# Kernel optimization log

Measured on AMD Instinct MI355X. Metric: run time of the kernel, lower is better.

The kernel has to match this reference:

```python
import jax, jax.numpy as jnp
import numpy as np

B, S, H = 2, 2048, 2048
NQ, NKV, D = 16, 4, 128
GROUPS = NQ // NKV
SCALE = 1.0 / np.sqrt(D).astype(np.float32)


def _make_rope(seq_len, dim, dtype=jnp.float32):
    inv_freq = 1.0 / (10000.0 ** (jnp.arange(0, dim, 2, dtype=jnp.float32) / dim))
    t = jnp.arange(seq_len, dtype=jnp.float32)
    freqs = jnp.outer(t, inv_freq)                      # [S, D/2]
    emb = jnp.concatenate([freqs, freqs], axis=-1)      # [S, D]
    cos = jnp.cos(emb).astype(dtype)[None, :, None, :]  # [1, S, 1, D]
    sin = jnp.sin(emb).astype(dtype)[None, :, None, :]
    return jnp.broadcast_to(cos, (B, seq_len, 1, dim)), jnp.broadcast_to(sin, (B, seq_len, 1, dim))


def _rotate_half(x):
    x1, x2 = jnp.split(x, 2, axis=-1)
    return jnp.concatenate([-x2, x1], axis=-1)


def _apply_rope(x, cos, sin):
    # x: [B, S, Hh, D]; cos/sin: [B, S, 1, D]
    return x * cos + _rotate_half(x) * sin


def setup_inputs() -> dict:
    key = jax.random.key(0)
    ks = jax.random.split(key, 8)
    x = jax.random.normal(ks[0], (B, S, H), dtype=jnp.float32)
    rope_cos, rope_sin = _make_rope(S, D)
    std = 1.0 / np.sqrt(H)
    Wq = jax.random.normal(ks[1], (NQ * D, H), dtype=jnp.float32) * std
    bq = jax.random.normal(ks[2], (NQ * D,), dtype=jnp.float32) * 0.01
    Wk = jax.random.normal(ks[3], (NKV * D, H), dtype=jnp.float32) * std
    bk = jax.random.normal(ks[4], (NKV * D,), dtype=jnp.float32) * 0.01
    Wv = jax.random.normal(ks[5], (NKV * D, H), dtype=jnp.float32) * std
    bv = jax.random.normal(ks[6], (NKV * D,), dtype=jnp.float32) * 0.01
    Wo = jax.random.normal(ks[7], (H, NQ * D), dtype=jnp.float32) * (1.0 / np.sqrt(NQ * D))
    return {"x": x, "rope_cos": rope_cos, "rope_sin": rope_sin,
            "Wq": Wq, "bq": bq, "Wk": Wk, "bk": bk, "Wv": Wv, "bv": bv, "Wo": Wo}


def reference(x, rope_cos, rope_sin, Wq, bq, Wk, bk, Wv, bv, Wo):
    Bx, Sx, _ = x.shape
    q = (x @ Wq.T + bq).reshape(Bx, Sx, NQ, D)
    k = (x @ Wk.T + bk).reshape(Bx, Sx, NKV, D)
    v = (x @ Wv.T + bv).reshape(Bx, Sx, NKV, D)
    q = _apply_rope(q, rope_cos, rope_sin)
    k = _apply_rope(k, rope_cos, rope_sin)
    q = q.transpose(0, 2, 1, 3)   # [B, NQ, S, D]
    k = k.transpose(0, 2, 1, 3)   # [B, NKV, S, D]
    v = v.transpose(0, 2, 1, 3)
    new_k, new_v = k, v           # kv cache (pre-repeat)
    kr = jnp.repeat(k, GROUPS, axis=1)  # [B, NQ, S_k, D]
    vr = jnp.repeat(v, GROUPS, axis=1)
    S_k = kr.shape[2]
    attn = jnp.einsum('bhsd,bhtd->bhst', q, kr) * SCALE
    row = jnp.arange(Sx)[:, None] + (S_k - Sx)
    col = jnp.arange(S_k)[None, :]
    mask = col > row                       # [S, S_k]
    attn = jnp.where(mask[None, None], -jnp.inf, attn)
    attn_max = jnp.max(attn, axis=-1, keepdims=True)
    attn = jnp.exp(attn - attn_max)
    attn = attn / (jnp.sum(attn, axis=-1, keepdims=True) + 1e-9)
    attn = jnp.nan_to_num(attn, nan=0.0)
    out = jnp.einsum('bhst,bhtd->bhsd', attn, vr)
    out = out.transpose(0, 2, 1, 3).reshape(Bx, Sx, NQ * D)
    out = out @ Wo.T
    return (out, new_k, new_v)
```

## Files before the change

kernel.cpp:

```cpp
#include <hip/hip_runtime.h>
#include <cstdint>
#include <cstddef>
#include <math.h>

constexpr int Bc   = 2;
constexpr int Sc   = 2048;
constexpr int Hc   = 2048;
constexpr int NQc  = 16;
constexpr int NKVc = 4;
constexpr int Dc   = 128;
#define SCALE_F 0.08838834764831845f

typedef __attribute__((ext_vector_type(8))) short  bf16x8;
typedef __attribute__((ext_vector_type(4))) float  f32x4;
typedef __attribute__((ext_vector_type(16))) float f32x16;

__device__ __forceinline__ uint16_t f2bf(float f) {
    union { float f; uint32_t u; } v; v.f = f;
    uint32_t u = v.u;
    return (uint16_t)((u + 0x7FFFu + ((u >> 16) & 1u)) >> 16);
}
__device__ __forceinline__ uint32_t pk2bf(float lo, float hi) {
    return (uint32_t)f2bf(lo) | ((uint32_t)f2bf(hi) << 16);
}
__device__ __forceinline__ float bfu2f(uint16_t u) {
    union { uint32_t u; float f; } v; v.u = (uint32_t)u << 16; return v.f;
}
__device__ __forceinline__ void lds_load16(void* lds, const void* g) {
    __builtin_amdgcn_global_load_lds(
        (const __attribute__((address_space(1))) uint32_t*)g,
        (__attribute__((address_space(3))) uint32_t*)lds, 16, 0, 0);
}
__device__ __forceinline__ bf16x8 mk8(uint32_t w0, uint32_t w1, uint32_t w2, uint32_t w3) {
    union { uint32_t u[4]; bf16x8 s; } t;
    t.u[0] = w0; t.u[1] = w1; t.u[2] = w2; t.u[3] = w3; return t.s;
}

__global__ __launch_bounds__(256) void cvt1_kernel(
    const float* __restrict__ x,  const float* __restrict__ wq,
    const float* __restrict__ wk, const float* __restrict__ wv,
    uint16_t* __restrict__ xb, uint16_t* __restrict__ wqkv)
{
    const long long TOT = 3670016LL;
    for (long long i = (long long)blockIdx.x * 256 + threadIdx.x; i < TOT;
         i += (long long)gridDim.x * 256) {
        const float* src; uint16_t* dst; long long off;
        if (i < 2097152LL)      { src = x;  dst = xb;             off = i; }
        else if (i < 3145728LL) { src = wq; dst = wqkv;           off = i - 2097152LL; }
        else if (i < 3407872LL) { src = wk; dst = wqkv + 4194304; off = i - 3145728LL; }
        else                    { src = wv; dst = wqkv + 5242880; off = i - 3407872LL; }
        float4 v = *((const float4*)src + off);
        uint2 o; o.x = pk2bf(v.x, v.y); o.y = pk2bf(v.z, v.w);
        *((uint2*)dst + off) = o;
    }
}

__global__ __launch_bounds__(256) void cvt2_kernel(
    const float* __restrict__ wo, uint16_t* __restrict__ wob)
{
    for (long long i = (long long)blockIdx.x * 256 + threadIdx.x; i < 1048576LL;
         i += (long long)gridDim.x * 256) {
        float4 v = *((const float4*)wo + i);
        uint2 o; o.x = pk2bf(v.x, v.y); o.y = pk2bf(v.z, v.w);
        *((uint2*)wob + i) = o;
    }
}

__device__ __forceinline__ void gemm_stage(const uint16_t* __restrict__ src,
                                           size_t row_stride, uint16_t* lds,
                                           int wid, int lane)
{
    #pragma unroll
    for (int i = 0; i < 4; ++i) {
        const int g = wid * 4 + i;
        const int r = g * 8 + (lane >> 3);
        const int slot = (lane & 7) ^ (r & 7);
        lds_load16(lds + g * 512, src + (size_t)r * row_stride + slot * 8);
    }
}

#define GEMM_CORE(AS, BS, AB, BB)                                              \
    f32x4 acc[4][4] = {};                                                      \
    gemm_stage(AB, 2048, &AS[0][0], wid, lane);                                \
    gemm_stage(BB, 2048, &BS[0][0], wid, lane);                                \
    __syncthreads();                                                           \
    for (int t = 0; t < 32; ++t) {                                             \
        const int cur = t & 1;                                                 \
        if (t + 1 < 32) {                                                      \
            gemm_stage(AB + (t + 1) * 64, 2048, &AS[cur ^ 1][0], wid, lane);   \
            gemm_stage(BB + (t + 1) * 64, 2048, &BS[cur ^ 1][0], wid, lane);   \
        }                                                                      \
        _Pragma("unroll")                                                      \
        for (int kk = 0; kk < 2; ++kk) {                                       \
            bf16x8 av[4], bw[4];                                               \
            _Pragma("unroll")                                                  \
            for (int mi = 0; mi < 4; ++mi) {                                   \
                const int row = wr * 64 + mi * 16 + (lane & 15);               \
                const int slot = (kk * 4 + (lane >> 4)) ^ (row & 7);           \
                av[mi] = *(const bf16x8*)&AS[cur][row * 64 + slot * 8];        \
            }                                                                  \
            _Pragma("unroll")                                                  \
            for (int nj = 0; nj < 4; ++nj) {                                   \
                const int row = wc * 64 + nj * 16 + (lane & 15);               \
                const int slot = (kk * 4 + (lane >> 4)) ^ (row & 7);           \
                bw[nj] = *(const bf16x8*)&BS[cur][row * 64 + slot * 8];        \
            }                                                                  \
            _Pragma("unroll")                                                  \
            for (int mi = 0; mi < 4; ++mi)                                     \
                _Pragma("unroll")                                              \
                for (int nj = 0; nj < 4; ++nj)                                 \
                    acc[mi][nj] = __builtin_amdgcn_mfma_f32_16x16x32_bf16(     \
                        av[mi], bw[nj], acc[mi][nj], 0, 0, 0);                 \
        }                                                                      \
        __syncthreads();                                                       \
    }

__global__ __launch_bounds__(256) void gemm_qkv_kernel(
    const uint16_t* __restrict__ xb, const uint16_t* __restrict__ wqkv,
    const float* __restrict__ bq, const float* __restrict__ bk, const float* __restrict__ bv,
    uint16_t* __restrict__ qb2, float* __restrict__ kbuf, float* __restrict__ vbuf)
{
    __shared__ __align__(16) uint16_t As[2][128 * 64];
    __shared__ __align__(16) uint16_t Bs[2][128 * 64];
    const int tid = threadIdx.x, lane = tid & 63, wid = tid >> 6;
    const int m0 = blockIdx.x * 128, n0 = blockIdx.y * 128;
    const int wr = wid >> 1, wc = wid & 1;
    const uint16_t* Ab = xb + (size_t)m0 * 2048;
    const uint16_t* Bb = wqkv + (size_t)n0 * 2048;

    GEMM_CORE(As, Bs, Ab, Bb)

    const float* bias; int rtype; int nbase;
    if (n0 < 2048)      { bias = bq + n0;          rtype = 0; nbase = n0; }
    else if (n0 < 2560) { bias = bk + (n0 - 2048); rtype = 1; nbase = n0 - 2048; }
    else                { bias = bv + (n0 - 2560); rtype = 2; nbase = n0 - 2560; }
    #pragma unroll
    for (int mi = 0; mi < 4; ++mi) {
        #pragma unroll
        for (int nj = 0; nj < 4; ++nj) {
            const int ct = wc * 64 + nj * 16 + (lane & 15);
            const int nloc = nbase + ct;
            const int head = nloc >> 7, d = nloc & 127;
            const float bval = bias[ct];
            #pragma unroll
            for (int j = 0; j < 4; ++j) {
                const int m = m0 + wr * 64 + mi * 16 + (lane >> 4) * 4 + j;
                const int bb2 = m >> 11, ss = m & 2047;
                const float v = acc[mi][nj][j] + bval;
                if (rtype == 0)
                    qb2[(((size_t)(bb2 * NQc + head) * Sc) + ss) * Dc + d] = f2bf(v);
                else if (rtype == 1)
                    kbuf[(((size_t)(bb2 * NKVc + head) * Sc) + ss) * Dc + d] = v;
                else
                    vbuf[(((size_t)(bb2 * NKVc + head) * Sc) + ss) * Dc + d] = v;
            }
        }
    }
}

__global__ __launch_bounds__(256) void gemm_out_kernel(
    const uint16_t* __restrict__ ab, const uint16_t* __restrict__ wob,
    float* __restrict__ C)
{
    __shared__ __align__(16) uint16_t As[2][128 * 64];
    __shared__ __align__(16) uint16_t Bs[2][128 * 64];
    const int tid = threadIdx.x, lane = tid & 63, wid = tid >> 6;
    const int m0 = blockIdx.x * 128, n0 = blockIdx.y * 128;
    const int wr = wid >> 1, wc = wid & 1;
    const uint16_t* Ab = ab + (size_t)m0 * 2048;
    const uint16_t* Bb = wob + (size_t)n0 * 2048;

    GEMM_CORE(As, Bs, Ab, Bb)

    #pragma unroll
    for (int mi = 0; mi < 4; ++mi) {
        #pragma unroll
        for (int nj = 0; nj < 4; ++nj) {
            const int n = n0 + wc * 64 + nj * 16 + (lane & 15);
            #pragma unroll
            for (int j = 0; j < 4; ++j) {
                const int m = m0 + wr * 64 + mi * 16 + (lane >> 4) * 4 + j;
                C[(size_t)m * 2048 + n] = acc[mi][nj][j];
            }
        }
    }
}

__global__ __launch_bounds__(256) void rope_kernel(
    uint16_t* __restrict__ qb2, float* __restrict__ kbuf,
    const float* __restrict__ cosb, const float* __restrict__ sinb,
    uint16_t* __restrict__ kb2)
{
    const int idx = blockIdx.x * 256 + threadIdx.x;
    const int e = idx & 31;
    int t = idx >> 5;
    const int ss = t & 2047; t >>= 11;
    const int h = t % 20, bb = t / 20;
    const float* cp = cosb + ((size_t)bb * Sc + ss) * Dc;
    const float* sp = sinb + ((size_t)bb * Sc + ss) * Dc;
    const float2 c1 = *(const float2*)(cp + 2 * e);
    const float2 c2 = *(const float2*)(cp + 64 + 2 * e);
    const float2 s1 = *(const float2*)(sp + 2 * e);
    const float2 s2 = *(const float2*)(sp + 64 + 2 * e);
    if (h < NQc) {
        const size_t base = (((size_t)(bb * NQc + h) * Sc) + ss) * Dc;
        const uint32_t u1 = *(const uint32_t*)(qb2 + base + 2 * e);
        const uint32_t u2 = *(const uint32_t*)(qb2 + base + 64 + 2 * e);
        const float x1a = bfu2f((uint16_t)u1), x1b = bfu2f((uint16_t)(u1 >> 16));
        const float x2a = bfu2f((uint16_t)u2), x2b = bfu2f((uint16_t)(u2 >> 16));
        const float lo0 = x1a * c1.x - x2a * s1.x, lo1 = x1b * c1.y - x2b * s1.y;
        const float hi0 = x2a * c2.x + x1a * s2.x, hi1 = x2b * c2.y + x1b * s2.y;
        *(uint32_t*)(qb2 + base + 2 * e)      = pk2bf(lo0, lo1);
        *(uint32_t*)(qb2 + base + 64 + 2 * e) = pk2bf(hi0, hi1);
    } else {
        const int hh = h - NQc;
        const size_t base = (((size_t)(bb * NKVc + hh) * Sc) + ss) * Dc;
        const float2 x1 = *(const float2*)(kbuf + base + 2 * e);
        const float2 x2 = *(const float2*)(kbuf + base + 64 + 2 * e);
        const float lo0 = x1.x * c1.x - x2.x * s1.x, lo1 = x1.y * c1.y - x2.y * s1.y;
        const float hi0 = x2.x * c2.x + x1.x * s2.x, hi1 = x2.y * c2.y + x1.y * s2.y;
        *(float2*)(kbuf + base + 2 * e)      = make_float2(lo0, lo1);
        *(float2*)(kbuf + base + 64 + 2 * e) = make_float2(hi0, hi1);
        *(uint32_t*)(kb2 + base + 2 * e)      = pk2bf(lo0, lo1);
        *(uint32_t*)(kb2 + base + 64 + 2 * e) = pk2bf(hi0, hi1);
    }
}

__global__ __launch_bounds__(256) void vtrans_kernel(
    const float* __restrict__ vbuf, uint16_t* __restrict__ vt)
{
    __shared__ uint16_t T[128][72];
    const int tid = threadIdx.x;
    const int st = blockIdx.x & 31;
    const int bh = blockIdx.x >> 5;
    const float* src = vbuf + ((size_t)bh * Sc + st * 64) * Dc;
    #pragma unroll
    for (int i = 0; i < 8; ++i) {
        const int f = tid + 256 * i;
        const int s_l = f >> 5, d4 = (f & 31) * 4;
        const float4 v = *((const float4*)(src + (size_t)s_l * Dc) + (f & 31));
        T[d4 + 0][s_l] = f2bf(v.x); T[d4 + 1][s_l] = f2bf(v.y);
        T[d4 + 2][s_l] = f2bf(v.z); T[d4 + 3][s_l] = f2bf(v.w);
    }
    __syncthreads();
    uint16_t* dst = vt + (size_t)bh * Dc * Sc + st * 64;
    #pragma unroll
    for (int i = 0; i < 8; ++i) {
        const int g = tid + 256 * i;
        const int d = g >> 4, s4 = (g & 15) * 4;
        *(uint2*)(dst + (size_t)d * Sc + s4) = *(const uint2*)&T[d][s4];
    }
}

__global__ __launch_bounds__(256, 2) void attn_kernel(
    const uint16_t* __restrict__ qb, const uint16_t* __restrict__ kb,
    const uint16_t* __restrict__ vt, uint16_t* __restrict__ ab)
{
    __shared__ __align__(16) uint16_t Ks[2][64 * 128];
    __shared__ __align__(16) uint16_t Vs[2][128 * 64];

    const int tid = threadIdx.x, lane = tid & 63, wid = tid >> 6;
    const int qt = 15 - blockIdx.x;
    const int bh = blockIdx.y;
    const int b = bh >> 4, h = bh & 15, hk = h >> 2;
    const int l31 = lane & 31, l5 = lane >> 5;

    const uint16_t* kpB = kb + ((size_t)(b * NKVc + hk) * Sc) * Dc;
    const uint16_t* vpB = vt + ((size_t)(b * NKVc + hk) * Dc) * Sc;

    const uint16_t* qbase =
        qb + (((size_t)(b * NQc + h) * Sc) + qt * 128 + wid * 32 + l31) * Dc;
    bf16x8 qf[8];
    #pragma unroll
    for (int kk = 0; kk < 8; ++kk)
        qf[kk] = *(const bf16x8*)(qbase + kk * 16 + l5 * 8);

    float m_r = -INFINITY, l_r = 0.f;
    f32x16 o0 = {}, o1 = {}, o2 = {}, o3 = {};

    const int qg = qt * 128 + wid * 32 + l31;
    const int NCH = 2 * qt + 2;

    auto stage = [&](int ch, int buf) {
        const int kb0 = ch * 64;
        #pragma unroll
        for (int i = 0; i < 4; ++i) {
            const int g = wid * 4 + i;
            const int row = g * 4 + (lane >> 4);
            const int slot = (lane & 15) ^ (row & 15);
            lds_load16(&Ks[buf][g * 512], kpB + (size_t)(kb0 + row) * Dc + slot * 8);
        }
        #pragma unroll
        for (int i = 0; i < 4; ++i) {
            const int g = wid * 4 + i;
            const int d = g * 8 + (lane >> 3);
            const int slot = (lane & 7) ^ (d & 7);
            lds_load16(&Vs[buf][g * 512], vpB + (size_t)d * Sc + kb0 + slot * 8);
        }
    };

    stage(0, 0);
    __syncthreads();

    for (int ch = 0; ch < NCH; ++ch) {
        const int buf = ch & 1;
        if (ch + 1 < NCH) stage(ch + 1, buf ^ 1);
        const int kb0 = ch * 64;

        f32x16 s0 = {}, s1 = {};
        #pragma unroll
        for (int kk = 0; kk < 8; ++kk) {
            const int r0 = l31;
            const int sl0 = (kk * 2 + l5) ^ (r0 & 15);
            const bf16x8 a0 = *(const bf16x8*)&Ks[buf][r0 * 128 + sl0 * 8];
            const int r1 = 32 + l31;
            const int sl1 = (kk * 2 + l5) ^ (r1 & 15);
            const bf16x8 a1 = *(const bf16x8*)&Ks[buf][r1 * 128 + sl1 * 8];
            s0 = __builtin_amdgcn_mfma_f32_32x32x16_bf16(a0, qf[kk], s0, 0, 0, 0);
            s1 = __builtin_amdgcn_mfma_f32_32x32x16_bf16(a1, qf[kk], s1, 0, 0, 0);
        }

        float p[32];
        float rm = -INFINITY;
        #pragma unroll
        for (int r = 0; r < 16; ++r) {
            const int krel = (r & 3) + 8 * (r >> 2) + 4 * l5;
            float v0 = s0[r] * SCALE_F;
            float v1 = s1[r] * SCALE_F;
            if (kb0 + krel > qg)      v0 = -INFINITY;
            if (kb0 + 32 + krel > qg) v1 = -INFINITY;
            p[r] = v0; p[16 + r] = v1;
            rm = fmaxf(rm, fmaxf(v0, v1));
        }
        rm = fmaxf(rm, __shfl_xor(rm, 32));
        const float mnew = fmaxf(m_r, rm);
        const float alpha = __expf(m_r - mnew);
        m_r = mnew;

        float sum = 0.f;
        uint32_t pb[16];
        #pragma unroll
        for (int j = 0; j < 8; ++j) {
            const float a0 = __expf(p[2 * j] - mnew),      a1 = __expf(p[2 * j + 1] - mnew);
            const float b0 = __expf(p[16 + 2 * j] - mnew), b1 = __expf(p[16 + 2 * j + 1] - mnew);
            sum += (a0 + a1) + (b0 + b1);
            pb[j]     = pk2bf(a0, a1);
            pb[8 + j] = pk2bf(b0, b1);
        }
        sum += __shfl_xor(sum, 32);
        l_r = l_r * alpha + sum;

        #pragma unroll
        for (int r = 0; r < 16; ++r) {
            const int qi = (r & 3) + 8 * (r >> 2) + 4 * l5;
            const float av = __shfl(alpha, qi);
            o0[r] *= av; o1[r] *= av; o2[r] *= av; o3[r] *= av;
        }

        uint32_t e[16];
        #pragma unroll
        for (int j = 0; j < 16; ++j) e[j] = __shfl_xor(pb[j], 32);
        const bool hi = (l5 == 1);
        const bf16x8 pa0 = hi ? mk8(e[2],  e[3],  pb[2],  pb[3])  : mk8(pb[0],  pb[1],  e[0],  e[1]);
        const bf16x8 pa1 = hi ? mk8(e[6],  e[7],  pb[6],  pb[7])  : mk8(pb[4],  pb[5],  e[4],  e[5]);
        const bf16x8 pa2 = hi ? mk8(e[10], e[11], pb[10], pb[11]) : mk8(pb[8],  pb[9],  e[8],  e[9]);
        const bf16x8 pa3 = hi ? mk8(e[14], e[15], pb[14], pb[15]) : mk8(pb[12], pb[13], e[12], e[13]);

        #define PV_DV(OO, DV)                                                        \
        {                                                                            \
            const int d = (DV) * 32 + l31;                                           \
            const int rb = d * 64; const int sw = d & 7;                             \
            const bf16x8 b0 = *(const bf16x8*)&Vs[buf][rb + ((0 * 2 + l5) ^ sw) * 8];\
            OO = __builtin_amdgcn_mfma_f32_32x32x16_bf16(pa0, b0, OO, 0, 0, 0);      \
            const bf16x8 b1 = *(const bf16x8*)&Vs[buf][rb + ((1 * 2 + l5) ^ sw) * 8];\
            OO = __builtin_amdgcn_mfma_f32_32x32x16_bf16(pa1, b1, OO, 0, 0, 0);      \
            const bf16x8 b2 = *(const bf16x8*)&Vs[buf][rb + ((2 * 2 + l5) ^ sw) * 8];\
            OO = __builtin_amdgcn_mfma_f32_32x32x16_bf16(pa2, b2, OO, 0, 0, 0);      \
            const bf16x8 b3 = *(const bf16x8*)&Vs[buf][rb + ((3 * 2 + l5) ^ sw) * 8];\
            OO = __builtin_amdgcn_mfma_f32_32x32x16_bf16(pa3, b3, OO, 0, 0, 0);      \
        }
        PV_DV(o0, 0) PV_DV(o1, 1) PV_DV(o2, 2) PV_DV(o3, 3)
        #undef PV_DV

        __syncthreads();
    }

    const float inv = 1.f / (l_r + 1e-9f);
    uint16_t* abase = ab + ((size_t)b * Sc) * 2048 + (size_t)h * Dc;
    #pragma unroll
    for (int r = 0; r < 16; ++r) {
        const int qi = (r & 3) + 8 * (r >> 2) + 4 * l5;
        const float iv = __shfl(inv, qi);
        const int srow = qt * 128 + wid * 32 + qi;
        uint16_t* dst = abase + (size_t)srow * 2048 + l31;
        dst[0]  = f2bf(o0[r] * iv);
        dst[32] = f2bf(o1[r] * iv);
        dst[64] = f2bf(o2[r] * iv);
        dst[96] = f2bf(o3[r] * iv);
    }
}

extern "C" void kernel_launch(void* const* d_in, const int* in_sizes, int n_in,
                              void* d_out, int out_size, void* d_ws, size_t ws_size,
                              hipStream_t stream)
{
    const float* x    = (const float*)d_in[0];
    const float* cosb = (const float*)d_in[1];
    const float* sinb = (const float*)d_in[2];
    const float* Wq   = (const float*)d_in[3];
    const float* bq   = (const float*)d_in[4];
    const float* Wk   = (const float*)d_in[5];
    const float* bk   = (const float*)d_in[6];
    const float* Wv   = (const float*)d_in[7];
    const float* bv   = (const float*)d_in[8];
    const float* Wo   = (const float*)d_in[9];

    float* out  = (float*)d_out;
    float* kout = out  + (size_t)Bc * Sc * Hc;
    float* vout = kout + (size_t)Bc * NKVc * Sc * Dc;
    uint16_t* qb2 = (uint16_t*)out;

    uint8_t* ws = (uint8_t*)d_ws;
    uint16_t* xb   = (uint16_t*)(ws);
    uint16_t* wqkv = (uint16_t*)(ws + (16u << 20));
    uint16_t* kb2  = (uint16_t*)(ws + (16u << 20));
    uint16_t* vb2t = (uint16_t*)(ws + (20u << 20));
    uint16_t* wob  = (uint16_t*)(ws + (24u << 20));
    uint16_t* ab   = (uint16_t*)(ws);

    cvt1_kernel<<<2048, 256, 0, stream>>>(x, Wq, Wk, Wv, xb, wqkv);

    gemm_qkv_kernel<<<dim3(32, 24), 256, 0, stream>>>(xb, wqkv, bq, bk, bv,
                                                      qb2, kout, vout);

    rope_kernel<<<10240, 256, 0, stream>>>(qb2, kout, cosb, sinb, kb2);

    vtrans_kernel<<<256, 256, 0, stream>>>(vout, vb2t);

    cvt2_kernel<<<1024, 256, 0, stream>>>(Wo, wob);

    attn_kernel<<<dim3(16, 32), 256, 0, stream>>>(qb2, kb2, vb2t, ab);

    gemm_out_kernel<<<dim3(32, 16), 256, 0, stream>>>(ab, wob, out);
}
```

Baseline: 381.4 us.

## Skip fully masked per-wave chunks, lazy rescale, exp2 softmax, permlane swap in attention

```diff
diff --git a/kernel.cpp b/kernel.cpp
--- a/kernel.cpp
+++ b/kernel.cpp
@@ -260,8 +260,10 @@
     __shared__ __align__(16) uint16_t Vs[2][128 * 64];
 
     const int tid = threadIdx.x, lane = tid & 63, wid = tid >> 6;
-    const int qt = 15 - blockIdx.x;
-    const int bh = blockIdx.y;
+    const int lin = blockIdx.x;
+    const int hf = lin >> 8, pp = lin & 255;
+    const int qt = hf ? (pp & 15) : (15 - (pp & 15));
+    const int bh = (pp >> 4) + hf * 16;
     const int b = bh >> 4, h = bh & 15, hk = h >> 2;
     const int l31 = lane & 31, l5 = lane >> 5;
 
@@ -278,8 +280,11 @@
     float m_r = -INFINITY, l_r = 0.f;
     f32x16 o0 = {}, o1 = {}, o2 = {}, o3 = {};
 
-    const int qg = qt * 128 + wid * 32 + l31;
+    const int qg      = qt * 128 + wid * 32 + l31;
+    const int qgw_min = qt * 128 + wid * 32;
+    const int qgw_max = qgw_min + 31;
     const int NCH = 2 * qt + 2;
+    constexpr float SCL2 = 0.08838834764831845f * 1.4426950408889634f;
 
     auto stage = [&](int ch, int buf) {
         const int kb0 = ch * 64;
@@ -307,80 +312,107 @@
         if (ch + 1 < NCH) stage(ch + 1, buf ^ 1);
         const int kb0 = ch * 64;
 
-        f32x16 s0 = {}, s1 = {};
-        #pragma unroll
-        for (int kk = 0; kk < 8; ++kk) {
-            const int r0 = l31;
-            const int sl0 = (kk * 2 + l5) ^ (r0 & 15);
-            const bf16x8 a0 = *(const bf16x8*)&Ks[buf][r0 * 128 + sl0 * 8];
-            const int r1 = 32 + l31;
-            const int sl1 = (kk * 2 + l5) ^ (r1 & 15);
-            const bf16x8 a1 = *(const bf16x8*)&Ks[buf][r1 * 128 + sl1 * 8];
-            s0 = __builtin_amdgcn_mfma_f32_32x32x16_bf16(a0, qf[kk], s0, 0, 0, 0);
-            s1 = __builtin_amdgcn_mfma_f32_32x32x16_bf16(a1, qf[kk], s1, 0, 0, 0);
+        if (kb0 <= qgw_max) {
+            f32x16 s0 = {}, s1 = {};
+            __builtin_amdgcn_s_setprio(1);
+            #pragma unroll
+            for (int kk = 0; kk < 8; ++kk) {
+                const int r0 = l31;
+                const int sl0 = (kk * 2 + l5) ^ (r0 & 15);
+                const bf16x8 a0 = *(const bf16x8*)&Ks[buf][r0 * 128 + sl0 * 8];
+                const int r1 = 32 + l31;
+                const int sl1 = (kk * 2 + l5) ^ (r1 & 15);
+                const bf16x8 a1 = *(const bf16x8*)&Ks[buf][r1 * 128 + sl1 * 8];
+                s0 = __builtin_amdgcn_mfma_f32_32x32x16_bf16(a0, qf[kk], s0, 0, 0, 0);
+                s1 = __builtin_amdgcn_mfma_f32_32x32x16_bf16(a1, qf[kk], s1, 0, 0, 0);
+            }
+            __builtin_amdgcn_s_setprio(0);
+
+            float p[32];
+            const bool needmask = (kb0 + 63 > qgw_min);
+            #pragma unroll
+            for (int r = 0; r < 16; ++r) {
+                float v0 = s0[r] * SCL2;
+                float v1 = s1[r] * SCL2;
+                if (needmask) {
+                    const int krel = (r & 3) + 8 * (r >> 2) + 4 * l5;
+                    if (kb0 + krel > qg)      v0 = -INFINITY;
+                    if (kb0 + 32 + krel > qg) v1 = -INFINITY;
+                }
+                p[r] = v0; p[16 + r] = v1;
+            }
+            float tm[16];
+            #pragma unroll
+            for (int i = 0; i < 16; ++i) tm[i] = fmaxf(p[i], p[16 + i]);
+            #pragma unroll
+            for (int i = 0; i < 8; ++i) tm[i] = fmaxf(tm[i], tm[8 + i]);
+            #pragma unroll
+            for (int i = 0; i < 4; ++i) tm[i] = fmaxf(tm[i], tm[4 + i]);
+            float rm = fmaxf(fmaxf(tm[0], tm[1]), fmaxf(tm[2], tm[3]));
+            rm = fmaxf(rm, __shfl_xor(rm, 32));
+
+            if (!__all(rm <= m_r + 8.0f)) {
+                const float mnew = fmaxf(m_r, rm);
+                const float alpha = exp2f(m_r - mnew);
+                #pragma unroll
+                for (int r = 0; r < 16; ++r) {
+                    const int qi = (r & 3) + 8 * (r >> 2) + 4 * l5;
+                    const float av = __shfl(alpha, qi);
+                    o0[r] *= av; o1[r] *= av; o2[r] *= av; o3[r] *= av;
+                }
+                l_r *= alpha;
+                m_r = mnew;
+            }
+
+            #pragma unroll
+            for (int j = 0; j < 32; ++j) p[j] = exp2f(p[j] - m_r);
+            float s8[8];
+            #pragma unroll
+            for (int i = 0; i < 8; ++i)
+                s8[i] = (p[i] + p[8 + i]) + (p[16 + i] + p[24 + i]);
+            float sum = ((s8[0] + s8[1]) + (s8[2] + s8[3]))
+                      + ((s8[4] + s8[5]) + (s8[6] + s8[7]));
+            sum += __shfl_xor(sum, 32);
+            l_r += sum;
+
+            uint32_t pb[16];
+            #pragma unroll
+            for (int j = 0; j < 8; ++j) {
+                asm("v_cvt_pk_bf16_f32 %0, %1, %2"
+                    : "=v"(pb[j]) : "v"(p[2 * j]), "v"(p[2 * j + 1]));
+                asm("v_cvt_pk_bf16_f32 %0, %1, %2"
+                    : "=v"(pb[8 + j]) : "v"(p[16 + 2 * j]), "v"(p[16 + 2 * j + 1]));
+            }
+            #pragma unroll
+            for (int g2 = 0; g2 < 4; ++g2) {
+                asm("v_permlane32_swap_b32 %0, %1"
+                    : "+v"(pb[4 * g2 + 0]), "+v"(pb[4 * g2 + 2]));
+                asm("v_permlane32_swap_b32 %0, %1"
+                    : "+v"(pb[4 * g2 + 1]), "+v"(pb[4 * g2 + 3]));
+            }
+            const bf16x8 pa0 = mk8(pb[0],  pb[1],  pb[2],  pb[3]);
+            const bf16x8 pa1 = mk8(pb[4],  pb[5],  pb[6],  pb[7]);
+            const bf16x8 pa2 = mk8(pb[8],  pb[9],  pb[10], pb[11]);
+            const bf16x8 pa3 = mk8(pb[12], pb[13], pb[14], pb[15]);
+
+            __builtin_amdgcn_s_setprio(1);
+            #define PV_DV(OO, DV)                                                        \
+            {                                                                            \
+                const int d = (DV) * 32 + l31;                                           \
+                const int rb = d * 64; const int sw = d & 7;                             \
+                const bf16x8 b0 = *(const bf16x8*)&Vs[buf][rb + ((0 * 2 + l5) ^ sw) * 8];\
+                OO = __builtin_amdgcn_mfma_f32_32x32x16_bf16(pa0, b0, OO, 0, 0, 0);      \
+                const bf16x8 b1 = *(const bf16x8*)&Vs[buf][rb + ((1 * 2 + l5) ^ sw) * 8];\
+                OO = __builtin_amdgcn_mfma_f32_32x32x16_bf16(pa1, b1, OO, 0, 0, 0);      \
+                const bf16x8 b2 = *(const bf16x8*)&Vs[buf][rb + ((2 * 2 + l5) ^ sw) * 8];\
+                OO = __builtin_amdgcn_mfma_f32_32x32x16_bf16(pa2, b2, OO, 0, 0, 0);      \
+                const bf16x8 b3 = *(const bf16x8*)&Vs[buf][rb + ((3 * 2 + l5) ^ sw) * 8];\
+                OO = __builtin_amdgcn_mfma_f32_32x32x16_bf16(pa3, b3, OO, 0, 0, 0);      \
+            }
+            PV_DV(o0, 0) PV_DV(o1, 1) PV_DV(o2, 2) PV_DV(o3, 3)
+            #undef PV_DV
+            __builtin_amdgcn_s_setprio(0);
         }
-
-        float p[32];
-        float rm = -INFINITY;
-        #pragma unroll
-        for (int r = 0; r < 16; ++r) {
-            const int krel = (r & 3) + 8 * (r >> 2) + 4 * l5;
-            float v0 = s0[r] * SCALE_F;
-            float v1 = s1[r] * SCALE_F;
-            if (kb0 + krel > qg)      v0 = -INFINITY;
-            if (kb0 + 32 + krel > qg) v1 = -INFINITY;
-            p[r] = v0; p[16 + r] = v1;
-            rm = fmaxf(rm, fmaxf(v0, v1));
-        }
-        rm = fmaxf(rm, __shfl_xor(rm, 32));
-        const float mnew = fmaxf(m_r, rm);
-        const float alpha = __expf(m_r - mnew);
-        m_r = mnew;
-
-        float sum = 0.f;
-        uint32_t pb[16];
-        #pragma unroll
-        for (int j = 0; j < 8; ++j) {
-            const float a0 = __expf(p[2 * j] - mnew),      a1 = __expf(p[2 * j + 1] - mnew);
-            const float b0 = __expf(p[16 + 2 * j] - mnew), b1 = __expf(p[16 + 2 * j + 1] - mnew);
-            sum += (a0 + a1) + (b0 + b1);
-            pb[j]     = pk2bf(a0, a1);
-            pb[8 + j] = pk2bf(b0, b1);
-        }
-        sum += __shfl_xor(sum, 32);
-        l_r = l_r * alpha + sum;
-
-        #pragma unroll
-        for (int r = 0; r < 16; ++r) {
-            const int qi = (r & 3) + 8 * (r >> 2) + 4 * l5;
-            const float av = __shfl(alpha, qi);
-            o0[r] *= av; o1[r] *= av; o2[r] *= av; o3[r] *= av;
-        }
-
-        uint32_t e[16];
-        #pragma unroll
-        for (int j = 0; j < 16; ++j) e[j] = __shfl_xor(pb[j], 32);
-        const bool hi = (l5 == 1);
-        const bf16x8 pa0 = hi ? mk8(e[2],  e[3],  pb[2],  pb[3])  : mk8(pb[0],  pb[1],  e[0],  e[1]);
-        const bf16x8 pa1 = hi ? mk8(e[6],  e[7],  pb[6],  pb[7])  : mk8(pb[4],  pb[5],  e[4],  e[5]);
-        const bf16x8 pa2 = hi ? mk8(e[10], e[11], pb[10], pb[11]) : mk8(pb[8],  pb[9],  e[8],  e[9]);
-        const bf16x8 pa3 = hi ? mk8(e[14], e[15], pb[14], pb[15]) : mk8(pb[12], pb[13], e[12], e[13]);
-
-        #define PV_DV(OO, DV)                                                        \
-        {                                                                            \
-            const int d = (DV) * 32 + l31;                                           \
-            const int rb = d * 64; const int sw = d & 7;                             \
-            const bf16x8 b0 = *(const bf16x8*)&Vs[buf][rb + ((0 * 2 + l5) ^ sw) * 8];\
-            OO = __builtin_amdgcn_mfma_f32_32x32x16_bf16(pa0, b0, OO, 0, 0, 0);      \
-            const bf16x8 b1 = *(const bf16x8*)&Vs[buf][rb + ((1 * 2 + l5) ^ sw) * 8];\
-            OO = __builtin_amdgcn_mfma_f32_32x32x16_bf16(pa1, b1, OO, 0, 0, 0);      \
-            const bf16x8 b2 = *(const bf16x8*)&Vs[buf][rb + ((2 * 2 + l5) ^ sw) * 8];\
-            OO = __builtin_amdgcn_mfma_f32_32x32x16_bf16(pa2, b2, OO, 0, 0, 0);      \
-            const bf16x8 b3 = *(const bf16x8*)&Vs[buf][rb + ((3 * 2 + l5) ^ sw) * 8];\
-            OO = __builtin_amdgcn_mfma_f32_32x32x16_bf16(pa3, b3, OO, 0, 0, 0);      \
-        }
-        PV_DV(o0, 0) PV_DV(o1, 1) PV_DV(o2, 2) PV_DV(o3, 3)
-        #undef PV_DV
 
         __syncthreads();
     }
@@ -439,7 +471,7 @@
 
     cvt2_kernel<<<1024, 256, 0, stream>>>(Wo, wob);
 
-    attn_kernel<<<dim3(16, 32), 256, 0, stream>>>(qb2, kb2, vb2t, ab);
+    attn_kernel<<<512, 256, 0, stream>>>(qb2, kb2, vb2t, ab);
 
     gemm_out_kernel<<<dim3(32, 16), 256, 0, stream>>>(ab, wob, out);
 }
```

Result: faster. 356.8 us (-6.5%).
